# Kernel optimization log

Measured on AMD Instinct MI355X. Metric: run time of the kernel, lower is better.

## Reference

```python
import jax, jax.numpy as jnp
import numpy as np

COMMITMENT_FACTOR = 0.25
QUANTIZATION_FACTOR = 1.0
KL_FACTOR = 0.0  # default kl_loss_factor


def setup_inputs() -> dict:
    key = jax.random.key(0)
    k1, k2 = jax.random.split(key)
    B, S, D, K = 4096, 8, 512, 4096
    z = jax.random.normal(k1, (B, S, D), dtype=jnp.float32)
    # codebook initialized ~ U(-1/sqrt(D), 1/sqrt(D)) in the original; scale accordingly
    embeddings = jax.random.uniform(k2, (K, D), dtype=jnp.float32,
                                    minval=-1.0 / np.sqrt(D), maxval=1.0 / np.sqrt(D))
    return {"z": z, "embeddings": embeddings}


def reference(z, embeddings):
    sg = jax.lax.stop_gradient
    D = z.shape[-1]
    K = embeddings.shape[0]
    zf = z.reshape(-1, D)  # [N, D]
    # squared euclidean distances via expansion: ||z||^2 + ||e||^2 - 2 z e^T  -> [N, K]
    distances = ((zf ** 2).sum(-1, keepdims=True)
                 + (embeddings ** 2).sum(-1)
                 - 2.0 * zf @ embeddings.T)
    closest = jnp.argmin(distances, axis=-1)  # [N]
    quantized_indices = closest.reshape(z.shape[:-1])  # [B, S]
    # one-hot @ codebook == gather
    quantized = embeddings[closest].reshape(z.shape)  # [B, S, D]

    commitment_loss = jnp.mean((sg(quantized) - z) ** 2)
    embedding_loss = jnp.mean((quantized - sg(z)) ** 2)
    # KL(uniform || softmax(-d)), batchmean over rows
    log_p = jax.nn.log_softmax(-distances, axis=-1)
    kl_loss = jnp.mean(jnp.sum((1.0 / K) * (-jnp.log(jnp.float32(K)) - log_p), axis=-1))

    loss = (commitment_loss * COMMITMENT_FACTOR
            + embedding_loss * QUANTIZATION_FACTOR
            + kl_loss * KL_FACTOR)
    # straight-through estimator (non-gumbel path)
    quantized_st = z + sg(quantized - z)
    return loss, quantized_st, quantized_indices
```

## Files before the change

kernel.cpp:

```cpp
#include <hip/hip_runtime.h>
#include <cstdint>
#include <cmath>

#define N_ROWS 32768
#define DIM    512
#define KCODES 4096
#define SPLITS 4
#define CPS    (KCODES / SPLITS)
#define KCL    (CPS / 64)
#define BM     128
#define TAU    2e-3f
#define CAP    1024
#define RQ     4

typedef _Float16 f16x8 __attribute__((ext_vector_type(8)));
typedef float    f32x4 __attribute__((ext_vector_type(4)));

#define OFF_NH  1048576
#define OFF_EN  (OFF_NH + KCODES)
#define OFF_R1  (OFF_EN + KCODES)
#define OFF_R2  (OFF_R1 + SPLITS * N_ROWS)
#define OFF_I1  (OFF_R2 + SPLITS * N_ROWS)
#define OFF_FI  (OFF_I1 + SPLITS * N_ROWS)
#define OFF_BI  (OFF_FI + N_ROWS)
#define OFF_BS  (OFF_BI + N_ROWS)
#define OFF_CT  (OFF_BS + 2048)
#define OFF_LR  (OFF_CT + 4)
#define OFF_LS  (OFF_LR + CAP)
#define OFF_SL  (OFF_LS + CAP)

__device__ __forceinline__ bool lexGT(float v1, int i1, float v2, int i2) {
  return (v1 > v2) || (v1 == v2 && i1 < i2);
}

__device__ __forceinline__ void gload16(const void* g, void* l) {
  __builtin_amdgcn_global_load_lds(
      (const __attribute__((address_space(1))) unsigned int*)g,
      (__attribute__((address_space(3))) unsigned int*)l, 16, 0, 0);
}

__device__ float np_sumsq_512(const float* __restrict__ a) {
#pragma clang fp contract(off)
  float B[4];
#pragma unroll
  for (int t = 0; t < 4; ++t) {
    const float* p = a + t * 128;
    float r[8];
    {
      float4 x0 = *(const float4*)p;
      float4 x1 = *(const float4*)(p + 4);
      r[0] = x0.x * x0.x; r[1] = x0.y * x0.y; r[2] = x0.z * x0.z; r[3] = x0.w * x0.w;
      r[4] = x1.x * x1.x; r[5] = x1.y * x1.y; r[6] = x1.z * x1.z; r[7] = x1.w * x1.w;
    }
    for (int i = 8; i < 128; i += 8) {
      float4 x0 = *(const float4*)(p + i);
      float4 x1 = *(const float4*)(p + i + 4);
      float f[8] = {x0.x, x0.y, x0.z, x0.w, x1.x, x1.y, x1.z, x1.w};
#pragma unroll
      for (int j = 0; j < 8; ++j) {
        float sq = f[j] * f[j];
        r[j] = r[j] + sq;
      }
    }
    B[t] = ((r[0] + r[1]) + (r[2] + r[3])) + ((r[4] + r[5]) + (r[6] + r[7]));
  }
  return (B[0] + B[1]) + (B[2] + B[3]);
}

__global__ __launch_bounds__(256) void vq_prep_e(const float* __restrict__ emb,
                                                 float* __restrict__ Enp,
                                                 float* __restrict__ negHalf,
                                                 int* __restrict__ counter) {
  if (blockIdx.x == 0 && threadIdx.x == 0) counter[0] = 0;
  int k = blockIdx.x * 256 + threadIdx.x;
  float E = np_sumsq_512(emb + (size_t)k * DIM);
  Enp[k] = E;
  negHalf[k] = -0.5f * E;
}

__global__ __launch_bounds__(256) void vq_prep_img(const float* __restrict__ emb,
                                                   f16x8* __restrict__ img) {
  int gid = blockIdx.x * 256 + threadIdx.x;
  int k = gid >> 6, seg = gid & 63;
  int dci = seg >> 4, s = seg & 15;
  int kcg = k >> 6, r = k & 63;
  int ct = r >> 4, tl = r & 15;
  int ks = s >> 2, gh = s & 3;
  int lane = gh * 16 + tl;
  const float* ep = emb + (size_t)k * DIM + dci * 128 + s * 8;
  float4 a = *(const float4*)ep;
  float4 b = *(const float4*)(ep + 4);
  float f[8] = {a.x, a.y, a.z, a.w, b.x, b.y, b.z, b.w};
  f16x8 h;
#pragma unroll
  for (int j = 0; j < 8; ++j) h[j] = (_Float16)f[j];
  img[(size_t)(kcg * 4 + dci) * 1024 + (ks * 4 + ct) * 64 + lane] = h;
}

__global__ __launch_bounds__(256, 2) void vq_main(const float* __restrict__ z,
                                                  const f16x8* __restrict__ img,
                                                  const float* __restrict__ negHalf,
                                                  float* __restrict__ R1s,
                                                  float* __restrict__ R2s,
                                                  int* __restrict__ I1s) {
  __shared__ f16x8 EHs[2048];

  const int tid  = threadIdx.x;
  const int w    = tid >> 6;
  const int lane = tid & 63;
  const int tl   = lane & 15;
  const int gh   = lane >> 4;
  const int bid  = blockIdx.x;
  const int rb   = bid >> 2;
  const int sp   = bid & 3;
  const int m0   = rb * BM;
  const int off  = (bid * 5) & (KCL - 1);

  f16x8 zh[2][16];
#pragma unroll
  for (int rt = 0; rt < 2; ++rt) {
    const float* zp = z + (size_t)(m0 + w * 32 + rt * 16 + tl) * DIM + gh * 8;
#pragma unroll
    for (int c = 0; c < 16; ++c) {
      float4 a = *(const float4*)(zp + c * 32);
      float4 b = *(const float4*)(zp + c * 32 + 4);
      float f[8] = {a.x, a.y, a.z, a.w, b.x, b.y, b.z, b.w};
      f16x8 h;
#pragma unroll
      for (int j = 0; j < 8; ++j) h[j] = (_Float16)f[j];
      zh[rt][c] = h;
    }
  }

  float R1[8], R2[8];
  int   I1u[8];
#pragma unroll
  for (int i = 0; i < 8; ++i) { R1[i] = -INFINITY; R2[i] = -INFINITY; I1u[i] = 0x7fffffff; }

  const f16x8* tbase = img + (size_t)sp * 64 * 1024;

  {
    const char* g = (const char*)(tbase + (size_t)(off * 4) * 1024) + w * 4096 + lane * 16;
    char* l = (char*)EHs + w * 4096;
#pragma unroll
    for (int i = 0; i < 4; ++i) gload16(g + i * 1024, l + i * 1024);
  }
  __syncthreads();

  for (int kclL = 0; kclL < KCL; ++kclL) {
    const int kcl = (kclL + off) & (KCL - 1);
    f32x4 acc[2][4];
#pragma unroll
    for (int ct = 0; ct < 4; ++ct) {
      float nh = negHalf[sp * CPS + kcl * 64 + ct * 16 + tl];
      acc[0][ct] = (f32x4){nh, nh, nh, nh};
      acc[1][ct] = (f32x4){nh, nh, nh, nh};
    }

#pragma unroll
    for (int dci = 0; dci < 4; ++dci) {
      const int t = kclL * 4 + dci;
      const int cur = t & 1;
      if (t + 1 < 64) {
        const int ndci = (dci + 1) & 3;
        const int nkcl = (dci == 3) ? ((kclL + 1 + off) & (KCL - 1)) : kcl;
        const char* g = (const char*)(tbase + (size_t)(nkcl * 4 + ndci) * 1024) + w * 4096 + lane * 16;
        char* l = (char*)EHs + (cur ^ 1) * 16384 + w * 4096;
#pragma unroll
        for (int i = 0; i < 4; ++i) gload16(g + i * 1024, l + i * 1024);
      }
      const f16x8* B = EHs + cur * 1024;
#pragma unroll
      for (int ks = 0; ks < 4; ++ks) {
        {
          f16x8 bf0 = B[(ks * 4 + 0) * 64 + lane];
          f16x8 bf1 = B[(ks * 4 + 1) * 64 + lane];
          acc[0][0] = __builtin_amdgcn_mfma_f32_16x16x32_f16(zh[0][dci * 4 + ks], bf0, acc[0][0], 0, 0, 0);
          acc[1][0] = __builtin_amdgcn_mfma_f32_16x16x32_f16(zh[1][dci * 4 + ks], bf0, acc[1][0], 0, 0, 0);
          acc[0][1] = __builtin_amdgcn_mfma_f32_16x16x32_f16(zh[0][dci * 4 + ks], bf1, acc[0][1], 0, 0, 0);
          acc[1][1] = __builtin_amdgcn_mfma_f32_16x16x32_f16(zh[1][dci * 4 + ks], bf1, acc[1][1], 0, 0, 0);
        }
        {
          f16x8 bf2 = B[(ks * 4 + 2) * 64 + lane];
          f16x8 bf3 = B[(ks * 4 + 3) * 64 + lane];
          acc[0][2] = __builtin_amdgcn_mfma_f32_16x16x32_f16(zh[0][dci * 4 + ks], bf2, acc[0][2], 0, 0, 0);
          acc[1][2] = __builtin_amdgcn_mfma_f32_16x16x32_f16(zh[1][dci * 4 + ks], bf2, acc[1][2], 0, 0, 0);
          acc[0][3] = __builtin_amdgcn_mfma_f32_16x16x32_f16(zh[0][dci * 4 + ks], bf3, acc[0][3], 0, 0, 0);
          acc[1][3] = __builtin_amdgcn_mfma_f32_16x16x32_f16(zh[1][dci * 4 + ks], bf3, acc[1][3], 0, 0, 0);
        }
      }
      __syncthreads();
    }

#pragma unroll
    for (int ct = 0; ct < 4; ++ct) {
      const int cu = sp * CPS + kcl * 64 + ct * 16;
#pragma unroll
      for (int rt = 0; rt < 2; ++rt)
#pragma unroll
        for (int i = 0; i < 4; ++i) {
          int r8 = rt * 4 + i;
          float v = acc[rt][ct][i];
          float u = fminf(v, R1[r8]);
          R2[r8] = fmaxf(u, R2[r8]);
          bool gt = v > R1[r8];
          R1[r8] = fmaxf(v, R1[r8]);
          I1u[r8] = gt ? cu : I1u[r8];
        }
    }
  }

  float R1f[8], R2f[8];
  int   I1f[8];
#pragma unroll
  for (int i = 0; i < 8; ++i) { R1f[i] = R1[i]; R2f[i] = R2[i]; I1f[i] = I1u[i] + tl; }

#pragma unroll
  for (int m = 1; m < 16; m <<= 1) {
#pragma unroll
    for (int i = 0; i < 8; ++i) {
      float o1 = __shfl_xor(R1f[i], m, 16);
      int   p1 = __shfl_xor(I1f[i], m, 16);
      float o2 = __shfl_xor(R2f[i], m, 16);
      R2f[i] = fmaxf(fmaxf(R2f[i], o2), fminf(R1f[i], o1));
      if (lexGT(o1, p1, R1f[i], I1f[i])) { R1f[i] = o1; I1f[i] = p1; }
    }
  }

  if (tl == 0) {
#pragma unroll
    for (int i = 0; i < 8; ++i) {
      int row = m0 + w * 32 + (i >> 2) * 16 + gh * 4 + (i & 3);
      R1s[(size_t)sp * N_ROWS + row] = R1f[i];
      R2s[(size_t)sp * N_ROWS + row] = R2f[i];
      I1s[(size_t)sp * N_ROWS + row] = I1f[i];
    }
  }
}

__global__ __launch_bounds__(256) void vq_merge(const float* __restrict__ z,
                                                const float* __restrict__ R1s,
                                                const float* __restrict__ R2s,
                                                const int* __restrict__ I1s,
                                                int* __restrict__ flagidx,
                                                int* __restrict__ bi,
                                                float* __restrict__ outIdx,
                                                int* __restrict__ counter,
                                                int* __restrict__ listRow,
                                                float* __restrict__ listS,
                                                unsigned long long* __restrict__ slots) {
  int row = blockIdx.x * 256 + threadIdx.x;
  float bR = -INFINITY, sec = -INFINITY;
  int bI = 0x7fffffff;
#pragma unroll
  for (int s = 0; s < 4; ++s) {
    float r1 = R1s[(size_t)s * N_ROWS + row];
    float r2 = R2s[(size_t)s * N_ROWS + row];
    int   i1 = I1s[(size_t)s * N_ROWS + row];
    sec = fmaxf(fmaxf(sec, r2), fminf(bR, r1));
    if (lexGT(r1, i1, bR, bI)) { bR = r1; bI = i1; }
  }
  bi[row] = bI;
  outIdx[row] = (float)bI;
  int fi = 0;
  if (bR - sec < TAU) {
#pragma clang fp contract(off)
    int pos = atomicAdd(counter, 1);
    if (pos < CAP) {
      listRow[pos] = row;
      listS[pos]   = np_sumsq_512(z + (size_t)row * DIM);
      slots[pos]   = ~0ull;
      fi = pos + 1;
    }
  }
  flagidx[row] = fi;
}

__global__ __launch_bounds__(256) void vq_rescan(const float* __restrict__ z,
                                                 const float* __restrict__ emb,
                                                 const float* __restrict__ Enp,
                                                 const int* __restrict__ counter,
                                                 const int* __restrict__ listRow,
                                                 const float* __restrict__ listS,
                                                 unsigned long long* __restrict__ slots) {
  __shared__ unsigned long long sred[4][RQ];
  const int tid = threadIdx.x;
  const int ci  = blockIdx.x & 15;
  const int gi  = blockIdx.x >> 4;
  const int c   = ci * 256 + tid;
  const float* er = emb + (size_t)c * DIM;
  const float En = Enp[c];
  int n = counter[0];
  if (n > CAP) n = CAP;
  for (int qt = gi * RQ; qt < n; qt += 64 * RQ) {
#pragma clang fp contract(off)
    int q0 = qt;
    int q1 = qt + 1 < n ? qt + 1 : n - 1;
    int q2 = qt + 2 < n ? qt + 2 : n - 1;
    int q3 = qt + 3 < n ? qt + 3 : n - 1;
    const float* zr0 = z + (size_t)listRow[q0] * DIM;
    const float* zr1 = z + (size_t)listRow[q1] * DIM;
    const float* zr2 = z + (size_t)listRow[q2] * DIM;
    const float* zr3 = z + (size_t)listRow[q3] * DIM;
    float a0 = 0.f, a1 = 0.f, a2 = 0.f, a3 = 0.f;
#pragma unroll 2
    for (int d0 = 0; d0 < DIM; d0 += 4) {
      float4 e  = *(const float4*)(er + d0);
      float4 x0 = *(const float4*)(zr0 + d0);
      float4 x1 = *(const float4*)(zr1 + d0);
      float4 x2 = *(const float4*)(zr2 + d0);
      float4 x3 = *(const float4*)(zr3 + d0);
      a0 = fmaf(x0.x, e.x, a0); a0 = fmaf(x0.y, e.y, a0);
      a0 = fmaf(x0.z, e.z, a0); a0 = fmaf(x0.w, e.w, a0);
      a1 = fmaf(x1.x, e.x, a1); a1 = fmaf(x1.y, e.y, a1);
      a1 = fmaf(x1.z, e.z, a1); a1 = fmaf(x1.w, e.w, a1);
      a2 = fmaf(x2.x, e.x, a2); a2 = fmaf(x2.y, e.y, a2);
      a2 = fmaf(x2.z, e.z, a2); a2 = fmaf(x2.w, e.w, a2);
      a3 = fmaf(x3.x, e.x, a3); a3 = fmaf(x3.y, e.y, a3);
      a3 = fmaf(x3.z, e.z, a3); a3 = fmaf(x3.w, e.w, a3);
    }
#pragma unroll
    for (int j = 0; j < RQ; ++j) {
      int   qj = (j == 0) ? q0 : (j == 1) ? q1 : (j == 2) ? q2 : q3;
      float aj = (j == 0) ? a0 : (j == 1) ? a1 : (j == 2) ? a2 : a3;
      float t = listS[qj] + En;
      float d = t - 2.0f * aj;
      unsigned long long p =
          ((unsigned long long)__builtin_bit_cast(unsigned int, d) << 32) | (unsigned int)c;
#pragma unroll
      for (int m = 1; m < 64; m <<= 1) {
        unsigned long long o = __shfl_xor(p, m, 64);
        p = o < p ? o : p;
      }
      if ((tid & 63) == 0) sred[tid >> 6][j] = p;
    }
    __syncthreads();
    if (tid < RQ) {
      int j = tid;
      int qj = (j == 0) ? q0 : (j == 1) ? q1 : (j == 2) ? q2 : q3;
      unsigned long long b = sred[0][j];
#pragma unroll
      for (int w2 = 1; w2 < 4; ++w2) b = sred[w2][j] < b ? sred[w2][j] : b;
      atomicMin(&slots[qj], b);
    }
    __syncthreads();
  }
}

__global__ __launch_bounds__(256) void vq_epi(const float* __restrict__ z,
                                              const float* __restrict__ emb,
                                              const int* __restrict__ bi,
                                              const int* __restrict__ flagidx,
                                              const unsigned long long* __restrict__ slots,
                                              float* __restrict__ out,
                                              float* __restrict__ outIdx,
                                              float* __restrict__ blockSums) {
  __shared__ float wred[4];
  int tid = threadIdx.x;
  int g = tid >> 4, tl = tid & 15;
  int row = blockIdx.x * 16 + g;
  int fi = flagidx[row];
  int code = bi[row];
  if (fi) {
    code = (int)(unsigned int)slots[fi - 1];
    if (tl == 0) outIdx[row] = (float)code;
  }
  const float* zr = z + (size_t)row * DIM;
  const float* er = emb + (size_t)code * DIM;
  float* oq = out + 1 + (size_t)row * DIM;
  float ls = 0.f;
#pragma unroll
  for (int j = 0; j < 8; ++j) {
    int d0 = (j * 16 + tl) * 4;
    float4 e = *(const float4*)(er + d0);
    float4 zz = *(const float4*)(zr + d0);
    float dx = e.x - zz.x, dy = e.y - zz.y, dz = e.z - zz.z, dw = e.w - zz.w;
    ls = fmaf(dx, dx, ls); ls = fmaf(dy, dy, ls);
    ls = fmaf(dz, dz, ls); ls = fmaf(dw, dw, ls);
    oq[d0 + 0] = e.x; oq[d0 + 1] = e.y; oq[d0 + 2] = e.z; oq[d0 + 3] = e.w;
  }
#pragma unroll
  for (int m = 1; m < 64; m <<= 1) ls += __shfl_xor(ls, m, 64);
  if ((tid & 63) == 0) wred[tid >> 6] = ls;
  __syncthreads();
  if (tid == 0) blockSums[blockIdx.x] = wred[0] + wred[1] + wred[2] + wred[3];
}

__global__ __launch_bounds__(256) void vq_final(const float* __restrict__ blockSums,
                                                float* __restrict__ out) {
  __shared__ float red[256];
  int t = threadIdx.x;
  float s = 0.f;
#pragma unroll
  for (int i = 0; i < 8; ++i) s += blockSums[t + i * 256];
  red[t] = s;
  __syncthreads();
  for (int k = 128; k > 0; k >>= 1) {
    if (t < k) red[t] += red[t + k];
    __syncthreads();
  }
  if (t == 0) out[0] = red[0] * (1.25f / 16777216.0f);
}

extern "C" void kernel_launch(void* const* d_in, const int* in_sizes, int n_in,
                              void* d_out, int out_size, void* d_ws, size_t ws_size,
                              hipStream_t stream) {
  const float* z   = (const float*)d_in[0];
  const float* emb = (const float*)d_in[1];
  float* out  = (float*)d_out;
  float* wsf  = (float*)d_ws;
  f16x8* img      = (f16x8*)d_ws;
  float* negHalf  = wsf + OFF_NH;
  float* Enp      = wsf + OFF_EN;
  float* R1s      = wsf + OFF_R1;
  float* R2s      = wsf + OFF_R2;
  int*   I1s      = (int*)(wsf + OFF_I1);
  int*   flagidx  = (int*)(wsf + OFF_FI);
  int*   bi       = (int*)(wsf + OFF_BI);
  float* bsums    = wsf + OFF_BS;
  int*   counter  = (int*)(wsf + OFF_CT);
  int*   listRow  = (int*)(wsf + OFF_LR);
  float* listS    = wsf + OFF_LS;
  unsigned long long* slots = (unsigned long long*)(wsf + OFF_SL);
  float* outIdx   = out + 1 + (size_t)N_ROWS * DIM;
  (void)in_sizes; (void)n_in; (void)out_size; (void)ws_size;

  vq_prep_e  <<<KCODES / 256, 256, 0, stream>>>(emb, Enp, negHalf, counter);
  vq_prep_img<<<1024, 256, 0, stream>>>(emb, img);
  vq_main    <<<1024, 256, 0, stream>>>(z, img, negHalf, R1s, R2s, I1s);
  vq_merge   <<<N_ROWS / 256, 256, 0, stream>>>(z, R1s, R2s, I1s, flagidx, bi, outIdx,
                                                counter, listRow, listS, slots);
  vq_rescan  <<<1024, 256, 0, stream>>>(z, emb, Enp, counter, listRow, listS, slots);
  vq_epi     <<<N_ROWS / 16, 256, 0, stream>>>(z, emb, bi, flagidx, slots, out, outIdx, bsums);
  vq_final   <<<1, 256, 0, stream>>>(bsums, out);
}
```

Measured before the change: 316.7 us.

## Stage half of codebook tile in LDS, read rest from global; fuse prep kernels

Halves the LDS staging buffer so only half of each codebook tile goes through shared memory, while the other half of the MFMA B operands is read straight from global/L2. The two prep kernels are merged into one launch, and the min-2-blocks launch bound on the main kernel is dropped. The intent is to cut LDS traffic and footprint and to save a launch. The risk is higher global-load latency inside the MFMA loop and different register/occupancy behaviour.

```diff
diff --git a/kernel.cpp b/kernel.cpp
--- a/kernel.cpp
+++ b/kernel.cpp
@@ -67,20 +67,18 @@
   return (B[0] + B[1]) + (B[2] + B[3]);
 }
 
-__global__ __launch_bounds__(256) void vq_prep_e(const float* __restrict__ emb,
-                                                 float* __restrict__ Enp,
-                                                 float* __restrict__ negHalf,
-                                                 int* __restrict__ counter) {
-  if (blockIdx.x == 0 && threadIdx.x == 0) counter[0] = 0;
-  int k = blockIdx.x * 256 + threadIdx.x;
-  float E = np_sumsq_512(emb + (size_t)k * DIM);
-  Enp[k] = E;
-  negHalf[k] = -0.5f * E;
-}
-
-__global__ __launch_bounds__(256) void vq_prep_img(const float* __restrict__ emb,
-                                                   f16x8* __restrict__ img) {
+__global__ __launch_bounds__(256) void vq_prep(const float* __restrict__ emb,
+                                               f16x8* __restrict__ img,
+                                               float* __restrict__ Enp,
+                                               float* __restrict__ negHalf,
+                                               int* __restrict__ counter) {
   int gid = blockIdx.x * 256 + threadIdx.x;
+  if (gid == 0) counter[0] = 0;
+  if (gid < KCODES) {
+    float E = np_sumsq_512(emb + (size_t)gid * DIM);
+    Enp[gid] = E;
+    negHalf[gid] = -0.5f * E;
+  }
   int k = gid >> 6, seg = gid & 63;
   int dci = seg >> 4, s = seg & 15;
   int kcg = k >> 6, r = k & 63;
@@ -97,13 +95,13 @@
   img[(size_t)(kcg * 4 + dci) * 1024 + (ks * 4 + ct) * 64 + lane] = h;
 }
 
-__global__ __launch_bounds__(256, 2) void vq_main(const float* __restrict__ z,
-                                                  const f16x8* __restrict__ img,
-                                                  const float* __restrict__ negHalf,
-                                                  float* __restrict__ R1s,
-                                                  float* __restrict__ R2s,
-                                                  int* __restrict__ I1s) {
-  __shared__ f16x8 EHs[2048];
+__global__ __launch_bounds__(256) void vq_main(const float* __restrict__ z,
+                                               const f16x8* __restrict__ img,
+                                               const float* __restrict__ negHalf,
+                                               float* __restrict__ R1s,
+                                               float* __restrict__ R2s,
+                                               int* __restrict__ I1s) {
+  __shared__ f16x8 EHs[1024];
 
   const int tid  = threadIdx.x;
   const int w    = tid >> 6;
@@ -139,12 +137,15 @@
 
   const f16x8* tbase = img + (size_t)sp * 64 * 1024;
 
-  {
-    const char* g = (const char*)(tbase + (size_t)(off * 4) * 1024) + w * 4096 + lane * 16;
-    char* l = (char*)EHs + w * 4096;
-#pragma unroll
-    for (int i = 0; i < 4; ++i) gload16(g + i * 1024, l + i * 1024);
-  }
+#define STAGE_HALF(pt_, buf_)                                                          \
+  {                                                                                    \
+    const char* g = (const char*)(tbase + (size_t)(pt_) * 1024) + w * 2048 + lane * 16;\
+    char* l = (char*)EHs + (buf_) * 8192 + w * 2048;                                   \
+    gload16(g, l);                                                                     \
+    gload16(g + 1024, l + 1024);                                                       \
+  }
+
+  STAGE_HALF(off * 4, 0);
   __syncthreads();
 
   for (int kclL = 0; kclL < KCL; ++kclL) {
@@ -161,33 +162,36 @@
     for (int dci = 0; dci < 4; ++dci) {
       const int t = kclL * 4 + dci;
       const int cur = t & 1;
+      const int pt = kcl * 4 + dci;
       if (t + 1 < 64) {
         const int ndci = (dci + 1) & 3;
         const int nkcl = (dci == 3) ? ((kclL + 1 + off) & (KCL - 1)) : kcl;
-        const char* g = (const char*)(tbase + (size_t)(nkcl * 4 + ndci) * 1024) + w * 4096 + lane * 16;
-        char* l = (char*)EHs + (cur ^ 1) * 16384 + w * 4096;
-#pragma unroll
-        for (int i = 0; i < 4; ++i) gload16(g + i * 1024, l + i * 1024);
+        STAGE_HALF(nkcl * 4 + ndci, cur ^ 1);
       }
-      const f16x8* B = EHs + cur * 1024;
+      const f16x8* B  = EHs + cur * 512;
+      const f16x8* Bg = tbase + (size_t)pt * 1024 + 512;
 #pragma unroll
       for (int ks = 0; ks < 4; ++ks) {
-        {
-          f16x8 bf0 = B[(ks * 4 + 0) * 64 + lane];
-          f16x8 bf1 = B[(ks * 4 + 1) * 64 + lane];
-          acc[0][0] = __builtin_amdgcn_mfma_f32_16x16x32_f16(zh[0][dci * 4 + ks], bf0, acc[0][0], 0, 0, 0);
-          acc[1][0] = __builtin_amdgcn_mfma_f32_16x16x32_f16(zh[1][dci * 4 + ks], bf0, acc[1][0], 0, 0, 0);
-          acc[0][1] = __builtin_amdgcn_mfma_f32_16x16x32_f16(zh[0][dci * 4 + ks], bf1, acc[0][1], 0, 0, 0);
-          acc[1][1] = __builtin_amdgcn_mfma_f32_16x16x32_f16(zh[1][dci * 4 + ks], bf1, acc[1][1], 0, 0, 0);
+        f16x8 bf0, bf1, bf2, bf3;
+        if (ks < 2) {
+          bf0 = B[(ks * 4 + 0) * 64 + lane];
+          bf1 = B[(ks * 4 + 1) * 64 + lane];
+          bf2 = B[(ks * 4 + 2) * 64 + lane];
+          bf3 = B[(ks * 4 + 3) * 64 + lane];
+        } else {
+          bf0 = Bg[((ks - 2) * 4 + 0) * 64 + lane];
+          bf1 = Bg[((ks - 2) * 4 + 1) * 64 + lane];
+          bf2 = Bg[((ks - 2) * 4 + 2) * 64 + lane];
+          bf3 = Bg[((ks - 2) * 4 + 3) * 64 + lane];
         }
-        {
-          f16x8 bf2 = B[(ks * 4 + 2) * 64 + lane];
-          f16x8 bf3 = B[(ks * 4 + 3) * 64 + lane];
-          acc[0][2] = __builtin_amdgcn_mfma_f32_16x16x32_f16(zh[0][dci * 4 + ks], bf2, acc[0][2], 0, 0, 0);
-          acc[1][2] = __builtin_amdgcn_mfma_f32_16x16x32_f16(zh[1][dci * 4 + ks], bf2, acc[1][2], 0, 0, 0);
-          acc[0][3] = __builtin_amdgcn_mfma_f32_16x16x32_f16(zh[0][dci * 4 + ks], bf3, acc[0][3], 0, 0, 0);
-          acc[1][3] = __builtin_amdgcn_mfma_f32_16x16x32_f16(zh[1][dci * 4 + ks], bf3, acc[1][3], 0, 0, 0);
-        }
+        acc[0][0] = __builtin_amdgcn_mfma_f32_16x16x32_f16(zh[0][dci * 4 + ks], bf0, acc[0][0], 0, 0, 0);
+        acc[1][0] = __builtin_amdgcn_mfma_f32_16x16x32_f16(zh[1][dci * 4 + ks], bf0, acc[1][0], 0, 0, 0);
+        acc[0][1] = __builtin_amdgcn_mfma_f32_16x16x32_f16(zh[0][dci * 4 + ks], bf1, acc[0][1], 0, 0, 0);
+        acc[1][1] = __builtin_amdgcn_mfma_f32_16x16x32_f16(zh[1][dci * 4 + ks], bf1, acc[1][1], 0, 0, 0);
+        acc[0][2] = __builtin_amdgcn_mfma_f32_16x16x32_f16(zh[0][dci * 4 + ks], bf2, acc[0][2], 0, 0, 0);
+        acc[1][2] = __builtin_amdgcn_mfma_f32_16x16x32_f16(zh[1][dci * 4 + ks], bf2, acc[1][2], 0, 0, 0);
+        acc[0][3] = __builtin_amdgcn_mfma_f32_16x16x32_f16(zh[0][dci * 4 + ks], bf3, acc[0][3], 0, 0, 0);
+        acc[1][3] = __builtin_amdgcn_mfma_f32_16x16x32_f16(zh[1][dci * 4 + ks], bf3, acc[1][3], 0, 0, 0);
       }
       __syncthreads();
     }
@@ -209,6 +213,7 @@
         }
     }
   }
+#undef STAGE_HALF
 
   float R1f[8], R2f[8];
   int   I1f[8];
@@ -425,8 +430,7 @@
   float* outIdx   = out + 1 + (size_t)N_ROWS * DIM;
   (void)in_sizes; (void)n_in; (void)out_size; (void)ws_size;
 
-  vq_prep_e  <<<KCODES / 256, 256, 0, stream>>>(emb, Enp, negHalf, counter);
-  vq_prep_img<<<1024, 256, 0, stream>>>(emb, img);
+  vq_prep    <<<1024, 256, 0, stream>>>(emb, img, Enp, negHalf, counter);
   vq_main    <<<1024, 256, 0, stream>>>(z, img, negHalf, R1s, R2s, I1s);
   vq_merge   <<<N_ROWS / 256, 256, 0, stream>>>(z, R1s, R2s, I1s, flagidx, bi, outIdx,
                                                 counter, listRow, listS, slots);
```

Result: slower. 342.8 us (+8.2%).

## Triple-buffer codebook tiles, cache negHalf in LDS, and merge prep kernels

Applied to the files above, without the earlier changes.

The main kernel's LDS staging goes from double to triple buffering with a prefetch distance of two tiles. The full __syncthreads is replaced by an explicit vmcnt wait plus s_barrier, so one tile's loads can stay in flight across the barrier. The per-tile negHalf global loads move into a block-wide LDS copy, the rotated per-block tile offset is dropped, and the launch_bounds occupancy hint of 2 is removed. The two prep kernels are fused into one launch. The gain is better hiding of load latency and less launch overhead, at the cost of more LDS (about 52KB), which may cut occupancy. Dropping the offset may also cause more L2 contention, since all blocks now read the same tiles at the same time.

```diff
diff --git a/kernel.cpp b/kernel.cpp
--- a/kernel.cpp
+++ b/kernel.cpp
@@ -67,20 +67,18 @@
   return (B[0] + B[1]) + (B[2] + B[3]);
 }
 
-__global__ __launch_bounds__(256) void vq_prep_e(const float* __restrict__ emb,
-                                                 float* __restrict__ Enp,
-                                                 float* __restrict__ negHalf,
-                                                 int* __restrict__ counter) {
-  if (blockIdx.x == 0 && threadIdx.x == 0) counter[0] = 0;
-  int k = blockIdx.x * 256 + threadIdx.x;
-  float E = np_sumsq_512(emb + (size_t)k * DIM);
-  Enp[k] = E;
-  negHalf[k] = -0.5f * E;
-}
-
-__global__ __launch_bounds__(256) void vq_prep_img(const float* __restrict__ emb,
-                                                   f16x8* __restrict__ img) {
+__global__ __launch_bounds__(256) void vq_prep(const float* __restrict__ emb,
+                                               f16x8* __restrict__ img,
+                                               float* __restrict__ Enp,
+                                               float* __restrict__ negHalf,
+                                               int* __restrict__ counter) {
   int gid = blockIdx.x * 256 + threadIdx.x;
+  if (gid == 0) counter[0] = 0;
+  if (gid < KCODES) {
+    float E = np_sumsq_512(emb + (size_t)gid * DIM);
+    Enp[gid] = E;
+    negHalf[gid] = -0.5f * E;
+  }
   int k = gid >> 6, seg = gid & 63;
   int dci = seg >> 4, s = seg & 15;
   int kcg = k >> 6, r = k & 63;
@@ -97,13 +95,14 @@
   img[(size_t)(kcg * 4 + dci) * 1024 + (ks * 4 + ct) * 64 + lane] = h;
 }
 
-__global__ __launch_bounds__(256, 2) void vq_main(const float* __restrict__ z,
-                                                  const f16x8* __restrict__ img,
-                                                  const float* __restrict__ negHalf,
-                                                  float* __restrict__ R1s,
-                                                  float* __restrict__ R2s,
-                                                  int* __restrict__ I1s) {
-  __shared__ f16x8 EHs[2048];
+__global__ __launch_bounds__(256) void vq_main(const float* __restrict__ z,
+                                               const f16x8* __restrict__ img,
+                                               const float* __restrict__ negHalf,
+                                               float* __restrict__ R1s,
+                                               float* __restrict__ R2s,
+                                               int* __restrict__ I1s) {
+  __shared__ f16x8 EHs[3 * 1024];
+  __shared__ float nhs[1024];
 
   const int tid  = threadIdx.x;
   const int w    = tid >> 6;
@@ -114,7 +113,6 @@
   const int rb   = bid >> 2;
   const int sp   = bid & 3;
   const int m0   = rb * BM;
-  const int off  = (bid * 5) & (KCL - 1);
 
   f16x8 zh[2][16];
 #pragma unroll
@@ -139,37 +137,39 @@
 
   const f16x8* tbase = img + (size_t)sp * 64 * 1024;
 
+#define STAGE(T_, b_)                                                              \
+  {                                                                                \
+    const char* g = (const char*)tbase + (size_t)(T_) * 16384 + w * 4096 + lane * 16; \
+    char* l = (char*)EHs + (b_) * 16384 + w * 4096;                                \
+    gload16(g, l);                                                                 \
+    gload16(g + 1024, l + 1024);                                                   \
+    gload16(g + 2048, l + 2048);                                                   \
+    gload16(g + 3072, l + 3072);                                                   \
+  }
+
   {
-    const char* g = (const char*)(tbase + (size_t)(off * 4) * 1024) + w * 4096 + lane * 16;
-    char* l = (char*)EHs + w * 4096;
-#pragma unroll
-    for (int i = 0; i < 4; ++i) gload16(g + i * 1024, l + i * 1024);
-  }
-  __syncthreads();
-
-  for (int kclL = 0; kclL < KCL; ++kclL) {
-    const int kcl = (kclL + off) & (KCL - 1);
+    float4 v = *(const float4*)&negHalf[sp * CPS + tid * 4];
+    *(float4*)&nhs[tid * 4] = v;
+  }
+  STAGE(0, 0);
+  STAGE(1, 1);
+  asm volatile("s_waitcnt vmcnt(4) lgkmcnt(0)" ::: "memory");
+  __builtin_amdgcn_s_barrier();
+
+  for (int kcl = 0; kcl < KCL; ++kcl) {
     f32x4 acc[2][4];
 #pragma unroll
     for (int ct = 0; ct < 4; ++ct) {
-      float nh = negHalf[sp * CPS + kcl * 64 + ct * 16 + tl];
+      float nh = nhs[kcl * 64 + ct * 16 + tl];
       acc[0][ct] = (f32x4){nh, nh, nh, nh};
       acc[1][ct] = (f32x4){nh, nh, nh, nh};
     }
 
 #pragma unroll
     for (int dci = 0; dci < 4; ++dci) {
-      const int t = kclL * 4 + dci;
-      const int cur = t & 1;
-      if (t + 1 < 64) {
-        const int ndci = (dci + 1) & 3;
-        const int nkcl = (dci == 3) ? ((kclL + 1 + off) & (KCL - 1)) : kcl;
-        const char* g = (const char*)(tbase + (size_t)(nkcl * 4 + ndci) * 1024) + w * 4096 + lane * 16;
-        char* l = (char*)EHs + (cur ^ 1) * 16384 + w * 4096;
-#pragma unroll
-        for (int i = 0; i < 4; ++i) gload16(g + i * 1024, l + i * 1024);
-      }
-      const f16x8* B = EHs + cur * 1024;
+      const int t = kcl * 4 + dci;
+      if (t + 2 < 64) STAGE(t + 2, (t + 2) % 3);
+      const f16x8* B = EHs + (t % 3) * 1024;
 #pragma unroll
       for (int ks = 0; ks < 4; ++ks) {
         {
@@ -189,7 +189,13 @@
           acc[1][3] = __builtin_amdgcn_mfma_f32_16x16x32_f16(zh[1][dci * 4 + ks], bf3, acc[1][3], 0, 0, 0);
         }
       }
-      __syncthreads();
+      if (t < 62) {
+        asm volatile("s_waitcnt vmcnt(4)" ::: "memory");
+        __builtin_amdgcn_s_barrier();
+      } else if (t == 62) {
+        asm volatile("s_waitcnt vmcnt(0)" ::: "memory");
+        __builtin_amdgcn_s_barrier();
+      }
     }
 
 #pragma unroll
@@ -209,6 +215,7 @@
         }
     }
   }
+#undef STAGE
 
   float R1f[8], R2f[8];
   int   I1f[8];
@@ -425,8 +432,7 @@
   float* outIdx   = out + 1 + (size_t)N_ROWS * DIM;
   (void)in_sizes; (void)n_in; (void)out_size; (void)ws_size;
 
-  vq_prep_e  <<<KCODES / 256, 256, 0, stream>>>(emb, Enp, negHalf, counter);
-  vq_prep_img<<<1024, 256, 0, stream>>>(emb, img);
+  vq_prep    <<<1024, 256, 0, stream>>>(emb, img, Enp, negHalf, counter);
   vq_main    <<<1024, 256, 0, stream>>>(z, img, negHalf, R1s, R2s, I1s);
   vq_merge   <<<N_ROWS / 256, 256, 0, stream>>>(z, R1s, R2s, I1s, flagidx, bi, outIdx,
                                                 counter, listRow, listS, slots);
```

New measurement: 328.7 us. +3.8%, slower.
